# Optimization experiments

Measured on AMD Instinct MI355X. Metric: run time of the kernel, lower is better.

## Reference

```python
import jax, jax.numpy as jnp
import numpy as np

B, S, H = 2, 2048, 2048
NQ, NKV = 32, 8
HD = H // NQ  # 64


def setup_inputs() -> dict:
    key = jax.random.key(0)
    ks = jax.random.split(key, 9)
    s = 1.0 / np.sqrt(H)
    return {
        "x": jax.random.normal(ks[0], (B, S, H), dtype=jnp.float32),
        "Wq": jax.random.normal(ks[1], (H, H), dtype=jnp.float32) * s,
        "bq": jnp.zeros((H,), dtype=jnp.float32),
        "Wk": jax.random.normal(ks[2], (H, NKV * HD), dtype=jnp.float32) * s,
        "bk": jnp.zeros((NKV * HD,), dtype=jnp.float32),
        "Wv": jax.random.normal(ks[3], (H, NKV * HD), dtype=jnp.float32) * s,
        "bv": jnp.zeros((NKV * HD,), dtype=jnp.float32),
        "Wo": jax.random.normal(ks[4], (H, H), dtype=jnp.float32) * s,
        "bo": jnp.zeros((H,), dtype=jnp.float32),
    }


def reference(x, Wq, bq, Wk, bk, Wv, bv, Wo, bo):
    Bx, Sx, _ = x.shape
    g = NQ // NKV  # queries per kv head
    q = (x @ Wq + bq).reshape(Bx, Sx, NKV, g, HD)   # grouped query heads
    k = (x @ Wk + bk).reshape(Bx, Sx, NKV, HD)
    v = (x @ Wv + bv).reshape(Bx, Sx, NKV, HD)
    # scores: [B, NKV, g, S, S] -- broadcast KV across group instead of jnp.repeat
    scores = jnp.einsum('bshgd,bkhd->bhgsk', q, k) / jnp.sqrt(jnp.float32(HD))
    probs = jax.nn.softmax(scores, axis=-1)
    out = jnp.einsum('bhgsk,bkhd->bshgd', probs, v).reshape(Bx, Sx, H)
    return out @ Wo + bo
```

## Files before the change

kernel.cpp:

```cpp
#include <hip/hip_runtime.h>
#include <cstdint>
#include <cstddef>

typedef unsigned short u16;
typedef __bf16 bf16x8 __attribute__((ext_vector_type(8)));
typedef float f32x4 __attribute__((ext_vector_type(4)));
typedef unsigned short u16x4 __attribute__((ext_vector_type(4)));
typedef unsigned short u16x8 __attribute__((ext_vector_type(8)));
typedef uint32_t u32x4 __attribute__((ext_vector_type(4)));
typedef __attribute__((address_space(1))) unsigned int as1_uint;
typedef __attribute__((address_space(3))) unsigned int as3_uint;

__device__ __forceinline__ u16 f2bf(float f) {
  uint32_t u = __builtin_bit_cast(uint32_t, f);
  u += 0x7FFFu + ((u >> 16) & 1u);
  return (u16)(u >> 16);
}

__device__ __forceinline__ uint32_t cvtpk2bf(float a, float b) {
  uint32_t r;
  asm("v_cvt_pk_bf16_f32 %0, %1, %2" : "=v"(r) : "v"(a), "v"(b));
  return r;
}

__device__ __forceinline__ float max3f(float a, float b, float c) {
  return fmaxf(fmaxf(a, b), c);
}

__device__ __forceinline__ void gld_lds16(const void* g, void* l) {
  __builtin_amdgcn_global_load_lds((as1_uint*)g, (as3_uint*)l, 16, 0, 0);
}

__global__ __launch_bounds__(256) void k_cast(const float* __restrict__ in,
                                              u16* __restrict__ out, int n8) {
  int i = blockIdx.x * 256 + threadIdx.x;
  if (i >= n8) return;
  const float4* p = reinterpret_cast<const float4*>(in) + (size_t)i * 2;
  float4 a = p[0], b = p[1];
  u16x8 r;
  r[0] = f2bf(a.x); r[1] = f2bf(a.y); r[2] = f2bf(a.z); r[3] = f2bf(a.w);
  r[4] = f2bf(b.x); r[5] = f2bf(b.y); r[6] = f2bf(b.z); r[7] = f2bf(b.w);
  *reinterpret_cast<u16x8*>(out + (size_t)i * 8) = r;
}

__global__ __launch_bounds__(256) void k_transpose_cast(const float* __restrict__ W,
                                                        u16* __restrict__ Wt,
                                                        int K, int N) {
  __shared__ u16 tile[64][72];
  int k0 = blockIdx.y * 64, n0 = blockIdx.x * 64;
  int r = threadIdx.x >> 4;
  int c4 = (threadIdx.x & 15) * 4;
#pragma unroll
  for (int i = 0; i < 4; ++i) {
    int kk = r + i * 16;
    float4 v = *reinterpret_cast<const float4*>(W + (size_t)(k0 + kk) * N + n0 + c4);
    tile[kk][c4 + 0] = f2bf(v.x); tile[kk][c4 + 1] = f2bf(v.y);
    tile[kk][c4 + 2] = f2bf(v.z); tile[kk][c4 + 3] = f2bf(v.w);
  }
  __syncthreads();
#pragma unroll
  for (int i = 0; i < 4; ++i) {
    int nn = r + i * 16;
    u16x4 o;
    o[0] = tile[c4 + 0][nn]; o[1] = tile[c4 + 1][nn];
    o[2] = tile[c4 + 2][nn]; o[3] = tile[c4 + 3][nn];
    *reinterpret_cast<u16x4*>(Wt + (size_t)(n0 + nn) * K + k0 + c4) = o;
  }
}

__global__ __launch_bounds__(256) void k_transpose_v(const u16* __restrict__ qkv,
                                                     u16* __restrict__ vt) {
  __shared__ u16 tile[64][72];
  const int t0 = blockIdx.x * 64, kvh = blockIdx.y, b = blockIdx.z;
  const u16* src = qkv + ((size_t)(b * 2048) + t0) * 3072 + 2560 + kvh * 64;
  u16* dst = vt + ((size_t)(b * 8 + kvh) * 64) * 2048 + t0;
  const int r = threadIdx.x >> 3;
  const int c8 = (threadIdx.x & 7) * 8;
#pragma unroll
  for (int i = 0; i < 2; ++i) {
    int rr = r + i * 32;
    u16x8 v = *reinterpret_cast<const u16x8*>(src + (size_t)rr * 3072 + c8);
#pragma unroll
    for (int j = 0; j < 8; ++j) tile[c8 + j][rr] = v[j];
  }
  __syncthreads();
#pragma unroll
  for (int i = 0; i < 2; ++i) {
    int rr = r + i * 32;
    u16x8 o;
#pragma unroll
    for (int j = 0; j < 8; ++j) o[j] = tile[rr][c8 + j];
    *reinterpret_cast<u16x8*>(dst + (size_t)rr * 2048 + c8) = o;
  }
}

__global__ __launch_bounds__(256) void k_concat_bias(const float* __restrict__ bq,
                                                     const float* __restrict__ bk,
                                                     const float* __restrict__ bv,
                                                     float* __restrict__ out) {
  int i = blockIdx.x * 256 + threadIdx.x;
  if (i >= 3072) return;
  float v;
  if (i < 2048) v = bq[i];
  else if (i < 2560) v = bk[i - 2048];
  else v = bv[i - 2560];
  out[i] = v;
}

template <bool F32OUT>
__global__ __launch_bounds__(256) void k_gemm(const u16* __restrict__ A,
                                              const u16* __restrict__ Bt,
                                              const float* __restrict__ bias,
                                              void* __restrict__ Cout,
                                              int M, int N, int K,
                                              int scaleN, float scaleV) {
  __shared__ __align__(16) u16 As[128 * 64];
  __shared__ __align__(16) u16 Bs[128 * 64];
  const int m0 = blockIdx.y * 128, n0 = blockIdx.x * 128;
  const int tid = threadIdx.x;
  const int l = tid & 63, w = tid >> 6;
  const int wm = w >> 1, wn = w & 1;
  const int lr = l & 15, lo = l >> 4;
  const int srow = w * 8 + (l >> 3);
  const int sc = (l & 7) ^ ((l >> 3) & 7);
  f32x4 acc[4][4] = {};
  for (int kt = 0; kt < K; kt += 64) {
    __syncthreads();
#pragma unroll
    for (int it = 0; it < 4; ++it) {
      int row = it * 32 + srow;
      gld_lds16(A + (size_t)(m0 + row) * K + kt + sc * 8,
                (char*)As + (it * 32 + w * 8) * 128);
      gld_lds16(Bt + (size_t)(n0 + row) * K + kt + sc * 8,
                (char*)Bs + (it * 32 + w * 8) * 128);
    }
    __syncthreads();
    bf16x8 af[4][2], bfr[4][2];
#pragma unroll
    for (int mi = 0; mi < 4; ++mi) {
      int row = wm * 64 + mi * 16 + lr;
#pragma unroll
      for (int ks = 0; ks < 2; ++ks) {
        int ch = (ks * 4 + lo) ^ (row & 7);
        af[mi][ks] = *reinterpret_cast<const bf16x8*>((const char*)As + row * 128 + ch * 16);
      }
    }
#pragma unroll
    for (int nj = 0; nj < 4; ++nj) {
      int row = wn * 64 + nj * 16 + lr;
#pragma unroll
      for (int ks = 0; ks < 2; ++ks) {
        int ch = (ks * 4 + lo) ^ (row & 7);
        bfr[nj][ks] = *reinterpret_cast<const bf16x8*>((const char*)Bs + row * 128 + ch * 16);
      }
    }
#pragma unroll
    for (int mi = 0; mi < 4; ++mi)
#pragma unroll
      for (int nj = 0; nj < 4; ++nj) {
        acc[mi][nj] = __builtin_amdgcn_mfma_f32_16x16x32_bf16(af[mi][0], bfr[nj][0], acc[mi][nj], 0, 0, 0);
        acc[mi][nj] = __builtin_amdgcn_mfma_f32_16x16x32_bf16(af[mi][1], bfr[nj][1], acc[mi][nj], 0, 0, 0);
      }
  }
#pragma unroll
  for (int mi = 0; mi < 4; ++mi) {
    int row = m0 + wm * 64 + mi * 16 + lo * 4;
#pragma unroll
    for (int nj = 0; nj < 4; ++nj) {
      int col = n0 + wn * 64 + nj * 16 + lr;
      float bv = bias[col];
      float scc = (col < scaleN) ? scaleV : 1.0f;
#pragma unroll
      for (int r = 0; r < 4; ++r) {
        float v = (acc[mi][nj][r] + bv) * scc;
        if (F32OUT) ((float*)Cout)[(size_t)(row + r) * N + col] = v;
        else        ((u16*)Cout)[(size_t)(row + r) * N + col] = f2bf(v);
      }
    }
  }
}

__global__ __launch_bounds__(256, 4) void k_attn(const u16* __restrict__ QKV,
                                                 const u16* __restrict__ VT,
                                                 u16* __restrict__ Oa) {
  constexpr int S = 2048, LDQ = 3072;
  constexpr float THR = 8.0f;
  __shared__ __align__(16) u16 Ks[2][64 * 64];
  __shared__ __align__(16) u16 Vs[2][64 * 64];
  const int qt = blockIdx.x, h = blockIdx.y, b = blockIdx.z;
  const int kvh = h >> 2;
  const int tid = threadIdx.x, l = tid & 63, w = tid >> 6;
  const int lr = l & 15, lo = l >> 4;
  const size_t base = (size_t)b * S * LDQ;
  const u16* Qg = QKV + base + h * 64;
  const u16* Kg = QKV + base + 2048 + kvh * 64;
  const u16* Vg = VT + (size_t)(b * 8 + kvh) * 64 * 2048;
  const int qrow = qt * 64 + w * 16 + lr;
  const bf16x8 aq0 = *reinterpret_cast<const bf16x8*>(Qg + (size_t)qrow * LDQ + lo * 8);
  const bf16x8 aq1 = *reinterpret_cast<const bf16x8*>(Qg + (size_t)qrow * LDQ + 32 + lo * 8);
  f32x4 acc[4] = {};
  float mrun = -1e30f, lsum = 0.f;
  const int krow = w * 8 + (l >> 3);
  const int ksc = (l & 7) ^ ((l >> 3) & 7);
  gld_lds16(Kg + (size_t)krow * LDQ + ksc * 8, (char*)Ks[0] + (w * 8) * 128);
  gld_lds16(Kg + (size_t)(32 + krow) * LDQ + ksc * 8, (char*)Ks[0] + (32 + w * 8) * 128);
  gld_lds16(Vg + (size_t)krow * 2048 + ksc * 8, (char*)Vs[0] + (w * 8) * 128);
  gld_lds16(Vg + (size_t)(32 + krow) * 2048 + ksc * 8, (char*)Vs[0] + (32 + w * 8) * 128);
  int cur = 0;
  for (int kt = 0; kt < S; kt += 64) {
    __syncthreads();
    if (kt + 64 < S) {
      const int nb = cur ^ 1, nk = kt + 64;
      gld_lds16(Kg + (size_t)(nk + krow) * LDQ + ksc * 8, (char*)Ks[nb] + (w * 8) * 128);
      gld_lds16(Kg + (size_t)(nk + 32 + krow) * LDQ + ksc * 8, (char*)Ks[nb] + (32 + w * 8) * 128);
      gld_lds16(Vg + (size_t)krow * 2048 + nk + ksc * 8, (char*)Vs[nb] + (w * 8) * 128);
      gld_lds16(Vg + (size_t)(32 + krow) * 2048 + nk + ksc * 8, (char*)Vs[nb] + (32 + w * 8) * 128);
    }
    float p[16];
    const u16* KsC = Ks[cur];
    __builtin_amdgcn_s_setprio(1);
#pragma unroll
    for (int t = 0; t < 4; ++t) {
      const int row = t * 16 + lr;
      bf16x8 k0 = *reinterpret_cast<const bf16x8*>((const char*)KsC + row * 128 + ((lo ^ (row & 7)) * 16));
      bf16x8 k1 = *reinterpret_cast<const bf16x8*>((const char*)KsC + row * 128 + (((4 + lo) ^ (row & 7)) * 16));
      f32x4 zz = {};
      zz = __builtin_amdgcn_mfma_f32_16x16x32_bf16(k0, aq0, zz, 0, 0, 0);
      zz = __builtin_amdgcn_mfma_f32_16x16x32_bf16(k1, aq1, zz, 0, 0, 0);
#pragma unroll
      for (int r = 0; r < 4; ++r) p[t * 4 + r] = zz[r];
    }
    __builtin_amdgcn_s_setprio(0);
    float m0 = max3f(p[0], p[1], p[2]);
    float m1 = max3f(p[3], p[4], p[5]);
    float m2 = max3f(p[6], p[7], p[8]);
    float m3 = max3f(p[9], p[10], p[11]);
    float m4 = max3f(p[12], p[13], p[14]);
    float tm = fmaxf(max3f(m0, m1, m2), max3f(m3, m4, p[15]));
    tm = fmaxf(tm, __shfl_xor(tm, 16, 64));
    tm = fmaxf(tm, __shfl_xor(tm, 32, 64));
    if (__all(tm <= mrun + THR)) {
#pragma unroll
      for (int i = 0; i < 16; ++i) p[i] = __builtin_amdgcn_exp2f(p[i] - mrun);
    } else {
      float mnew = fmaxf(mrun, tm);
      float alpha = __builtin_amdgcn_exp2f(mrun - mnew);
      mrun = mnew;
#pragma unroll
      for (int i = 0; i < 16; ++i) p[i] = __builtin_amdgcn_exp2f(p[i] - mnew);
      lsum *= alpha;
#pragma unroll
      for (int r = 0; r < 4; ++r) {
        float ar = __shfl(alpha, lo * 4 + r, 64);
#pragma unroll
        for (int nj = 0; nj < 4; ++nj) acc[nj][r] *= ar;
      }
    }
    float rs = (((p[0] + p[1]) + (p[2] + p[3])) + ((p[4] + p[5]) + (p[6] + p[7])))
             + (((p[8] + p[9]) + (p[10] + p[11])) + ((p[12] + p[13]) + (p[14] + p[15])));
    rs += __shfl_xor(rs, 16, 64);
    rs += __shfl_xor(rs, 32, 64);
    lsum += rs;
    uint32_t w00 = cvtpk2bf(p[0], p[1]),   w01 = cvtpk2bf(p[2], p[3]);
    uint32_t w10 = cvtpk2bf(p[4], p[5]),   w11 = cvtpk2bf(p[6], p[7]);
    uint32_t w20 = cvtpk2bf(p[8], p[9]),   w21 = cvtpk2bf(p[10], p[11]);
    uint32_t w30 = cvtpk2bf(p[12], p[13]), w31 = cvtpk2bf(p[14], p[15]);
    asm volatile("v_permlane32_swap_b32 %0, %1" : "+v"(w00), "+v"(w10));
    asm volatile("v_permlane16_swap_b32 %0, %1" : "+v"(w00), "+v"(w10));
    asm volatile("v_permlane32_swap_b32 %0, %1" : "+v"(w01), "+v"(w11));
    asm volatile("v_permlane16_swap_b32 %0, %1" : "+v"(w01), "+v"(w11));
    asm volatile("v_permlane32_swap_b32 %0, %1" : "+v"(w20), "+v"(w30));
    asm volatile("v_permlane16_swap_b32 %0, %1" : "+v"(w20), "+v"(w30));
    asm volatile("v_permlane32_swap_b32 %0, %1" : "+v"(w21), "+v"(w31));
    asm volatile("v_permlane16_swap_b32 %0, %1" : "+v"(w21), "+v"(w31));
    u32x4 pq0; pq0[0] = w00; pq0[1] = w01; pq0[2] = w10; pq0[3] = w11;
    u32x4 pq1; pq1[0] = w20; pq1[1] = w21; pq1[2] = w30; pq1[3] = w31;
    const bf16x8 pa0 = __builtin_bit_cast(bf16x8, pq0);
    const bf16x8 pa1 = __builtin_bit_cast(bf16x8, pq1);
    const u16* VsC = Vs[cur];
    __builtin_amdgcn_s_setprio(1);
#pragma unroll
    for (int nj = 0; nj < 4; ++nj) {
      const int vr = nj * 16 + lr;
      const bf16x8 bv0 = *reinterpret_cast<const bf16x8*>((const char*)VsC + vr * 128 + ((lo ^ (vr & 7)) * 16));
      const bf16x8 bv1 = *reinterpret_cast<const bf16x8*>((const char*)VsC + vr * 128 + (((4 + lo) ^ (vr & 7)) * 16));
      acc[nj] = __builtin_amdgcn_mfma_f32_16x16x32_bf16(pa0, bv0, acc[nj], 0, 0, 0);
      acc[nj] = __builtin_amdgcn_mfma_f32_16x16x32_bf16(pa1, bv1, acc[nj], 0, 0, 0);
    }
    __builtin_amdgcn_s_setprio(0);
    cur ^= 1;
  }
  float lf[4];
#pragma unroll
  for (int r = 0; r < 4; ++r) lf[r] = 1.0f / __shfl(lsum, lo * 4 + r, 64);
  const size_t orow = (size_t)b * S + qt * 64 + w * 16 + lo * 4;
#pragma unroll
  for (int nj = 0; nj < 4; ++nj) {
    const int col = h * 64 + nj * 16 + lr;
#pragma unroll
    for (int r = 0; r < 4; ++r)
      Oa[(orow + r) * 2048 + col] = f2bf(acc[nj][r] * lf[r]);
  }
}

extern "C" void kernel_launch(void* const* d_in, const int* in_sizes, int n_in,
                              void* d_out, int out_size, void* d_ws, size_t ws_size,
                              hipStream_t stream) {
  const float* x  = (const float*)d_in[0];
  const float* Wq = (const float*)d_in[1];
  const float* bq = (const float*)d_in[2];
  const float* Wk = (const float*)d_in[3];
  const float* bk = (const float*)d_in[4];
  const float* Wv = (const float*)d_in[5];
  const float* bv = (const float*)d_in[6];
  const float* Wo = (const float*)d_in[7];
  const float* bo = (const float*)d_in[8];
  float* out = (float*)d_out;
  char* ws = (char*)d_ws;

  u16*   xb    = (u16*)(ws + 0);
  u16*   vtg   = (u16*)(ws + 0);
  u16*   wqkvT = (u16*)(ws + 16777216);
  u16*   woT   = (u16*)(ws + 29360128);
  u16*   qkv   = (u16*)(ws + 37748736);
  u16*   attn  = (u16*)(ws + 62914560);
  float* bcat  = (float*)(ws + 79691776);

  const float SCL = 0.125f * 1.44269504088896341f;

  k_cast<<<4096, 256, 0, stream>>>(x, xb, 1048576);
  k_transpose_cast<<<dim3(32, 32), 256, 0, stream>>>(Wq, wqkvT, 2048, 2048);
  k_transpose_cast<<<dim3(8, 32), 256, 0, stream>>>(Wk, wqkvT + (size_t)2048 * 2048, 2048, 512);
  k_transpose_cast<<<dim3(8, 32), 256, 0, stream>>>(Wv, wqkvT + (size_t)2560 * 2048, 2048, 512);
  k_transpose_cast<<<dim3(32, 32), 256, 0, stream>>>(Wo, woT, 2048, 2048);
  k_concat_bias<<<12, 256, 0, stream>>>(bq, bk, bv, bcat);
  k_gemm<false><<<dim3(24, 32), 256, 0, stream>>>(xb, wqkvT, bcat, qkv, 4096, 3072, 2048, 2048, SCL);
  k_transpose_v<<<dim3(32, 8, 2), 256, 0, stream>>>(qkv, vtg);
  k_attn<<<dim3(32, 32, 2), 256, 0, stream>>>(qkv, vtg, attn);
  k_gemm<true><<<dim3(16, 32), 256, 0, stream>>>(attn, woT, bo, out, 4096, 2048, 2048, 0, 1.0f);
}
```

Before: 291.9 us.

## Process two query sub-tiles per wave in attention and remap GEMM block order

The attention kernel now has each wave handle 32 query rows as two 16-row sub-tiles, so each block covers 128 queries. Every K/V tile loaded into LDS is reused for twice as many MFMAs, and the grid is halved. The GEMM kernel also remaps block IDs in groups of 8, likely to spread neighbouring tiles across XCDs for better L2 locality. In exchange, register pressure rises in the attention kernel and there are fewer blocks (1024) to fill the GPU.

```diff
diff --git a/kernel.cpp b/kernel.cpp
--- a/kernel.cpp
+++ b/kernel.cpp
@@ -116,7 +116,10 @@
                                               int scaleN, float scaleV) {
   __shared__ __align__(16) u16 As[128 * 64];
   __shared__ __align__(16) u16 Bs[128 * 64];
-  const int m0 = blockIdx.y * 128, n0 = blockIdx.x * 128;
+  const int id = blockIdx.y * gridDim.x + blockIdx.x;
+  const int cpx = (gridDim.x * gridDim.y) >> 3;
+  const int nid = (id & 7) * cpx + (id >> 3);
+  const int m0 = (nid / gridDim.x) * 128, n0 = (nid % gridDim.x) * 128;
   const int tid = threadIdx.x;
   const int l = tid & 63, w = tid >> 6;
   const int wm = w >> 1, wn = w & 1;
@@ -180,11 +183,60 @@
   }
 }
 
+__device__ __forceinline__ void softmax_pack(float (&p)[16], float& mrun, float& lsum,
+                                             f32x4 (&acc)[4], int lo,
+                                             u32x4& pq0, u32x4& pq1) {
+  constexpr float THR = 8.0f;
+  float m0 = max3f(p[0], p[1], p[2]);
+  float m1 = max3f(p[3], p[4], p[5]);
+  float m2 = max3f(p[6], p[7], p[8]);
+  float m3 = max3f(p[9], p[10], p[11]);
+  float m4 = max3f(p[12], p[13], p[14]);
+  float tm = fmaxf(max3f(m0, m1, m2), max3f(m3, m4, p[15]));
+  tm = fmaxf(tm, __shfl_xor(tm, 16, 64));
+  tm = fmaxf(tm, __shfl_xor(tm, 32, 64));
+  if (__all(tm <= mrun + THR)) {
+#pragma unroll
+    for (int i = 0; i < 16; ++i) p[i] = __builtin_amdgcn_exp2f(p[i] - mrun);
+  } else {
+    float mnew = fmaxf(mrun, tm);
+    float alpha = __builtin_amdgcn_exp2f(mrun - mnew);
+    mrun = mnew;
+#pragma unroll
+    for (int i = 0; i < 16; ++i) p[i] = __builtin_amdgcn_exp2f(p[i] - mnew);
+    lsum *= alpha;
+#pragma unroll
+    for (int r = 0; r < 4; ++r) {
+      float ar = __shfl(alpha, lo * 4 + r, 64);
+#pragma unroll
+      for (int nj = 0; nj < 4; ++nj) acc[nj][r] *= ar;
+    }
+  }
+  float rs = (((p[0] + p[1]) + (p[2] + p[3])) + ((p[4] + p[5]) + (p[6] + p[7])))
+           + (((p[8] + p[9]) + (p[10] + p[11])) + ((p[12] + p[13]) + (p[14] + p[15])));
+  rs += __shfl_xor(rs, 16, 64);
+  rs += __shfl_xor(rs, 32, 64);
+  lsum += rs;
+  uint32_t w00 = cvtpk2bf(p[0], p[1]),   w01 = cvtpk2bf(p[2], p[3]);
+  uint32_t w10 = cvtpk2bf(p[4], p[5]),   w11 = cvtpk2bf(p[6], p[7]);
+  uint32_t w20 = cvtpk2bf(p[8], p[9]),   w21 = cvtpk2bf(p[10], p[11]);
+  uint32_t w30 = cvtpk2bf(p[12], p[13]), w31 = cvtpk2bf(p[14], p[15]);
+  asm volatile("v_permlane32_swap_b32 %0, %1" : "+v"(w00), "+v"(w10));
+  asm volatile("v_permlane16_swap_b32 %0, %1" : "+v"(w00), "+v"(w10));
+  asm volatile("v_permlane32_swap_b32 %0, %1" : "+v"(w01), "+v"(w11));
+  asm volatile("v_permlane16_swap_b32 %0, %1" : "+v"(w01), "+v"(w11));
+  asm volatile("v_permlane32_swap_b32 %0, %1" : "+v"(w20), "+v"(w30));
+  asm volatile("v_permlane16_swap_b32 %0, %1" : "+v"(w20), "+v"(w30));
+  asm volatile("v_permlane32_swap_b32 %0, %1" : "+v"(w21), "+v"(w31));
+  asm volatile("v_permlane16_swap_b32 %0, %1" : "+v"(w21), "+v"(w31));
+  pq0[0] = w00; pq0[1] = w01; pq0[2] = w10; pq0[3] = w11;
+  pq1[0] = w20; pq1[1] = w21; pq1[2] = w30; pq1[3] = w31;
+}
+
 __global__ __launch_bounds__(256, 4) void k_attn(const u16* __restrict__ QKV,
                                                  const u16* __restrict__ VT,
                                                  u16* __restrict__ Oa) {
   constexpr int S = 2048, LDQ = 3072;
-  constexpr float THR = 8.0f;
   __shared__ __align__(16) u16 Ks[2][64 * 64];
   __shared__ __align__(16) u16 Vs[2][64 * 64];
   const int qt = blockIdx.x, h = blockIdx.y, b = blockIdx.z;
@@ -195,11 +247,13 @@
   const u16* Qg = QKV + base + h * 64;
   const u16* Kg = QKV + base + 2048 + kvh * 64;
   const u16* Vg = VT + (size_t)(b * 8 + kvh) * 64 * 2048;
-  const int qrow = qt * 64 + w * 16 + lr;
-  const bf16x8 aq0 = *reinterpret_cast<const bf16x8*>(Qg + (size_t)qrow * LDQ + lo * 8);
-  const bf16x8 aq1 = *reinterpret_cast<const bf16x8*>(Qg + (size_t)qrow * LDQ + 32 + lo * 8);
-  f32x4 acc[4] = {};
-  float mrun = -1e30f, lsum = 0.f;
+  const int qrow0 = qt * 128 + w * 32 + lr;
+  const bf16x8 aq0 = *reinterpret_cast<const bf16x8*>(Qg + (size_t)qrow0 * LDQ + lo * 8);
+  const bf16x8 aq1 = *reinterpret_cast<const bf16x8*>(Qg + (size_t)qrow0 * LDQ + 32 + lo * 8);
+  const bf16x8 aq2 = *reinterpret_cast<const bf16x8*>(Qg + (size_t)(qrow0 + 16) * LDQ + lo * 8);
+  const bf16x8 aq3 = *reinterpret_cast<const bf16x8*>(Qg + (size_t)(qrow0 + 16) * LDQ + 32 + lo * 8);
+  f32x4 acc0[4] = {}, acc1[4] = {};
+  float mrun0 = -1e30f, lsum0 = 0.f, mrun1 = -1e30f, lsum1 = 0.f;
   const int krow = w * 8 + (l >> 3);
   const int ksc = (l & 7) ^ ((l >> 3) & 7);
   gld_lds16(Kg + (size_t)krow * LDQ + ksc * 8, (char*)Ks[0] + (w * 8) * 128);
@@ -216,7 +270,7 @@
       gld_lds16(Vg + (size_t)krow * 2048 + nk + ksc * 8, (char*)Vs[nb] + (w * 8) * 128);
       gld_lds16(Vg + (size_t)(32 + krow) * 2048 + nk + ksc * 8, (char*)Vs[nb] + (32 + w * 8) * 128);
     }
-    float p[16];
+    float p0[16], p1[16];
     const u16* KsC = Ks[cur];
     __builtin_amdgcn_s_setprio(1);
 #pragma unroll
@@ -224,59 +278,22 @@
       const int row = t * 16 + lr;
       bf16x8 k0 = *reinterpret_cast<const bf16x8*>((const char*)KsC + row * 128 + ((lo ^ (row & 7)) * 16));
       bf16x8 k1 = *reinterpret_cast<const bf16x8*>((const char*)KsC + row * 128 + (((4 + lo) ^ (row & 7)) * 16));
-      f32x4 zz = {};
-      zz = __builtin_amdgcn_mfma_f32_16x16x32_bf16(k0, aq0, zz, 0, 0, 0);
-      zz = __builtin_amdgcn_mfma_f32_16x16x32_bf16(k1, aq1, zz, 0, 0, 0);
-#pragma unroll
-      for (int r = 0; r < 4; ++r) p[t * 4 + r] = zz[r];
+      f32x4 z0 = {}, z1 = {};
+      z0 = __builtin_amdgcn_mfma_f32_16x16x32_bf16(k0, aq0, z0, 0, 0, 0);
+      z0 = __builtin_amdgcn_mfma_f32_16x16x32_bf16(k1, aq1, z0, 0, 0, 0);
+      z1 = __builtin_amdgcn_mfma_f32_16x16x32_bf16(k0, aq2, z1, 0, 0, 0);
+      z1 = __builtin_amdgcn_mfma_f32_16x16x32_bf16(k1, aq3, z1, 0, 0, 0);
+#pragma unroll
+      for (int r = 0; r < 4; ++r) { p0[t * 4 + r] = z0[r]; p1[t * 4 + r] = z1[r]; }
     }
     __builtin_amdgcn_s_setprio(0);
-    float m0 = max3f(p[0], p[1], p[2]);
-    float m1 = max3f(p[3], p[4], p[5]);
-    float m2 = max3f(p[6], p[7], p[8]);
-    float m3 = max3f(p[9], p[10], p[11]);
-    float m4 = max3f(p[12], p[13], p[14]);
-    float tm = fmaxf(max3f(m0, m1, m2), max3f(m3, m4, p[15]));
-    tm = fmaxf(tm, __shfl_xor(tm, 16, 64));
-    tm = fmaxf(tm, __shfl_xor(tm, 32, 64));
-    if (__all(tm <= mrun + THR)) {
-#pragma unroll
-      for (int i = 0; i < 16; ++i) p[i] = __builtin_amdgcn_exp2f(p[i] - mrun);
-    } else {
-      float mnew = fmaxf(mrun, tm);
-      float alpha = __builtin_amdgcn_exp2f(mrun - mnew);
-      mrun = mnew;
-#pragma unroll
-      for (int i = 0; i < 16; ++i) p[i] = __builtin_amdgcn_exp2f(p[i] - mnew);
-      lsum *= alpha;
-#pragma unroll
-      for (int r = 0; r < 4; ++r) {
-        float ar = __shfl(alpha, lo * 4 + r, 64);
-#pragma unroll
-        for (int nj = 0; nj < 4; ++nj) acc[nj][r] *= ar;
-      }
-    }
-    float rs = (((p[0] + p[1]) + (p[2] + p[3])) + ((p[4] + p[5]) + (p[6] + p[7])))
-             + (((p[8] + p[9]) + (p[10] + p[11])) + ((p[12] + p[13]) + (p[14] + p[15])));
-    rs += __shfl_xor(rs, 16, 64);
-    rs += __shfl_xor(rs, 32, 64);
-    lsum += rs;
-    uint32_t w00 = cvtpk2bf(p[0], p[1]),   w01 = cvtpk2bf(p[2], p[3]);
-    uint32_t w10 = cvtpk2bf(p[4], p[5]),   w11 = cvtpk2bf(p[6], p[7]);
-    uint32_t w20 = cvtpk2bf(p[8], p[9]),   w21 = cvtpk2bf(p[10], p[11]);
-    uint32_t w30 = cvtpk2bf(p[12], p[13]), w31 = cvtpk2bf(p[14], p[15]);
-    asm volatile("v_permlane32_swap_b32 %0, %1" : "+v"(w00), "+v"(w10));
-    asm volatile("v_permlane16_swap_b32 %0, %1" : "+v"(w00), "+v"(w10));
-    asm volatile("v_permlane32_swap_b32 %0, %1" : "+v"(w01), "+v"(w11));
-    asm volatile("v_permlane16_swap_b32 %0, %1" : "+v"(w01), "+v"(w11));
-    asm volatile("v_permlane32_swap_b32 %0, %1" : "+v"(w20), "+v"(w30));
-    asm volatile("v_permlane16_swap_b32 %0, %1" : "+v"(w20), "+v"(w30));
-    asm volatile("v_permlane32_swap_b32 %0, %1" : "+v"(w21), "+v"(w31));
-    asm volatile("v_permlane16_swap_b32 %0, %1" : "+v"(w21), "+v"(w31));
-    u32x4 pq0; pq0[0] = w00; pq0[1] = w01; pq0[2] = w10; pq0[3] = w11;
-    u32x4 pq1; pq1[0] = w20; pq1[1] = w21; pq1[2] = w30; pq1[3] = w31;
+    u32x4 pq0, pq1, pq2, pq3;
+    softmax_pack(p0, mrun0, lsum0, acc0, lo, pq0, pq1);
+    softmax_pack(p1, mrun1, lsum1, acc1, lo, pq2, pq3);
     const bf16x8 pa0 = __builtin_bit_cast(bf16x8, pq0);
     const bf16x8 pa1 = __builtin_bit_cast(bf16x8, pq1);
+    const bf16x8 pa2 = __builtin_bit_cast(bf16x8, pq2);
+    const bf16x8 pa3 = __builtin_bit_cast(bf16x8, pq3);
     const u16* VsC = Vs[cur];
     __builtin_amdgcn_s_setprio(1);
 #pragma unroll
@@ -284,22 +301,29 @@
       const int vr = nj * 16 + lr;
       const bf16x8 bv0 = *reinterpret_cast<const bf16x8*>((const char*)VsC + vr * 128 + ((lo ^ (vr & 7)) * 16));
       const bf16x8 bv1 = *reinterpret_cast<const bf16x8*>((const char*)VsC + vr * 128 + (((4 + lo) ^ (vr & 7)) * 16));
-      acc[nj] = __builtin_amdgcn_mfma_f32_16x16x32_bf16(pa0, bv0, acc[nj], 0, 0, 0);
-      acc[nj] = __builtin_amdgcn_mfma_f32_16x16x32_bf16(pa1, bv1, acc[nj], 0, 0, 0);
+      acc0[nj] = __builtin_amdgcn_mfma_f32_16x16x32_bf16(pa0, bv0, acc0[nj], 0, 0, 0);
+      acc0[nj] = __builtin_amdgcn_mfma_f32_16x16x32_bf16(pa1, bv1, acc0[nj], 0, 0, 0);
+      acc1[nj] = __builtin_amdgcn_mfma_f32_16x16x32_bf16(pa2, bv0, acc1[nj], 0, 0, 0);
+      acc1[nj] = __builtin_amdgcn_mfma_f32_16x16x32_bf16(pa3, bv1, acc1[nj], 0, 0, 0);
     }
     __builtin_amdgcn_s_setprio(0);
     cur ^= 1;
   }
-  float lf[4];
-#pragma unroll
-  for (int r = 0; r < 4; ++r) lf[r] = 1.0f / __shfl(lsum, lo * 4 + r, 64);
-  const size_t orow = (size_t)b * S + qt * 64 + w * 16 + lo * 4;
+  float lf0[4], lf1[4];
+#pragma unroll
+  for (int r = 0; r < 4; ++r) {
+    lf0[r] = 1.0f / __shfl(lsum0, lo * 4 + r, 64);
+    lf1[r] = 1.0f / __shfl(lsum1, lo * 4 + r, 64);
+  }
+  const size_t orow0 = (size_t)b * S + qt * 128 + w * 32 + lo * 4;
 #pragma unroll
   for (int nj = 0; nj < 4; ++nj) {
     const int col = h * 64 + nj * 16 + lr;
 #pragma unroll
-    for (int r = 0; r < 4; ++r)
-      Oa[(orow + r) * 2048 + col] = f2bf(acc[nj][r] * lf[r]);
+    for (int r = 0; r < 4; ++r) {
+      Oa[(orow0 + r) * 2048 + col] = f2bf(acc0[nj][r] * lf0[r]);
+      Oa[(orow0 + 16 + r) * 2048 + col] = f2bf(acc1[nj][r] * lf1[r]);
+    }
   }
 }
 
@@ -336,6 +360,6 @@
   k_concat_bias<<<12, 256, 0, stream>>>(bq, bk, bv, bcat);
   k_gemm<false><<<dim3(24, 32), 256, 0, stream>>>(xb, wqkvT, bcat, qkv, 4096, 3072, 2048, 2048, SCL);
   k_transpose_v<<<dim3(32, 8, 2), 256, 0, stream>>>(qkv, vtg);
-  k_attn<<<dim3(32, 32, 2), 256, 0, stream>>>(qkv, vtg, attn);
+  k_attn<<<dim3(16, 32, 2), 256, 0, stream>>>(qkv, vtg, attn);
   k_gemm<true><<<dim3(16, 32), 256, 0, stream>>>(attn, woT, bo, out, 4096, 2048, 2048, 0, 1.0f);
 }
```

Result: slower. 304.3 us (+4.3%).
